# Kernel optimization log

Hardware: AMD Instinct MI355X
Metric: run time of the kernel (lower is better)

The kernel has to match this reference:

```python
import jax, jax.numpy as jnp
import numpy as np

E = 100      # embedding_dim
FS = 5       # filter_size
HS = 6       # hidden_size (conv output spatial)
D1, D2 = 10, 10  # emb_dim1, emb_dim2
RD = E * FS * FS  # relation_dim = 2500
NE = 100000  # num_entities
NR = 500     # num_relations
B = 256      # batch
EPS = 1e-5


def _bn(x, g, b, m, v, axis):
    shape = [1] * x.ndim
    shape[axis] = x.shape[axis]
    g, b, m, v = (t.reshape(shape) for t in (g, b, m, v))
    return (x - m) * jax.lax.rsqrt(v + EPS) * g + b


def setup_inputs() -> dict:
    key = jax.random.key(0)
    ks = jax.random.split(key, 24)
    def bn_params(k, n):
        k1, k2 = jax.random.split(k)
        return (jnp.ones((n,), jnp.float32),                       # gamma
                jnp.zeros((n,), jnp.float32),                      # beta
                0.1 * jax.random.normal(k1, (n,), jnp.float32),    # running mean
                jax.random.uniform(k2, (n,), jnp.float32, 0.5, 1.5))  # running var
    bn_rel = bn_params(ks[0], RD)
    bn0 = bn_params(ks[1], 1)
    bn1 = bn_params(ks[2], E)
    bn2 = bn_params(ks[3], E)
    inp = {
        'emb_e': jax.random.normal(ks[4], (NE, E), jnp.float32),
        'emb_rel': jax.random.normal(ks[5], (NR, RD), jnp.float32) * 0.1,
        'bn_rel_g': bn_rel[0], 'bn_rel_b': bn_rel[1], 'bn_rel_m': bn_rel[2], 'bn_rel_v': bn_rel[3],
        'bn0_g': bn0[0], 'bn0_b': bn0[1], 'bn0_m': bn0[2], 'bn0_v': bn0[3],
        'bn1_g': bn1[0], 'bn1_b': bn1[1], 'bn1_m': bn1[2], 'bn1_v': bn1[3],
        'fc_w': jax.random.normal(ks[6], (E * HS * HS, E), jnp.float32) / np.sqrt(E * HS * HS),
        'fc_b': jnp.zeros((E,), jnp.float32),
        'bn2_g': bn2[0], 'bn2_b': bn2[1], 'bn2_m': bn2[2], 'bn2_v': bn2[3],
        'bias': jnp.zeros((NE,), jnp.float32),
        'e1': jax.random.randint(ks[7], (B,), 0, NE),
        'rel': jax.random.randint(ks[8], (B,), 0, NR),
    }
    return inp


def reference(emb_e, emb_rel, bn_rel_g, bn_rel_b, bn_rel_m, bn_rel_v,
              bn0_g, bn0_b, bn0_m, bn0_v, bn1_g, bn1_b, bn1_m, bn1_v,
              fc_w, fc_b, bn2_g, bn2_b, bn2_m, bn2_v, bias, e1, rel):
    # entity embedding -> (B, 1, 10, 10)
    e1_emb = emb_e[e1].reshape(B, 1, D1, D2)
    # relation embedding -> per-sample conv filters
    r = emb_rel[rel]                                   # (B, 2500)
    r = _bn(r, bn_rel_g, bn_rel_b, bn_rel_m, bn_rel_v, axis=1)
    x0 = _bn(e1_emb, bn0_g, bn0_b, bn0_m, bn0_v, axis=1)
    filters = r.reshape(B, E, FS * FS)                 # (B, 100, 25)
    # per-sample dynamic-filter conv as one batched contraction over patches
    patches = jax.lax.conv_general_dilated_patches(
        x0, (FS, FS), (1, 1), 'VALID')                 # (B, 25, 6, 6)
    x = jnp.einsum('bkhw,bck->bchw', patches, filters)  # (B, 100, 6, 6)
    x = jax.nn.relu(_bn(x, bn1_g, bn1_b, bn1_m, bn1_v, axis=1))
    x = x.reshape(B, -1)                               # (B, 3600)
    x = x @ fc_w + fc_b                                # (B, 100)
    x = jax.nn.relu(_bn(x, bn2_g, bn2_b, bn2_m, bn2_v, axis=1))
    scores = x @ emb_e.T + bias                        # (B, NE)
    return jax.nn.sigmoid(scores)
```

## Files before the change

kernel.cpp:

```cpp
#include <hip/hip_runtime.h>
#include <hip/hip_bf16.h>
#include <hip/hip_fp16.h>

#define EPS 1e-5f
#define NE_ 100000
#define B_  256

typedef _Float16 half8 __attribute__((ext_vector_type(8)));
typedef float floatx16 __attribute__((ext_vector_type(16)));

#define WS_X1    0
#define WS_PART  921600
#define WS_H16   1331200

__global__ __launch_bounds__(256) void k_conv(
    const float* __restrict__ emb_e,
    const float* __restrict__ emb_rel,
    const float* __restrict__ bnr_g, const float* __restrict__ bnr_b,
    const float* __restrict__ bnr_m, const float* __restrict__ bnr_v,
    const float* __restrict__ bn0_g, const float* __restrict__ bn0_b,
    const float* __restrict__ bn0_m, const float* __restrict__ bn0_v,
    const float* __restrict__ bn1_g, const float* __restrict__ bn1_b,
    const float* __restrict__ bn1_m, const float* __restrict__ bn1_v,
    const int* __restrict__ e1, const int* __restrict__ rel,
    float* __restrict__ x1)
{
    __shared__ float x0s[100];
    __shared__ float fs[2500];

    const int b = blockIdx.x;
    const int t = threadIdx.x;
    const int ei = e1[b];
    const int ri = rel[b];

    if (t < 100) {
        float sc = bn0_g[0] * rsqrtf(bn0_v[0] + EPS);
        float sh = bn0_b[0] - bn0_m[0] * sc;
        x0s[t] = emb_e[(size_t)ei * 100 + t] * sc + sh;
    }
    for (int j = t; j < 2500; j += 256) {
        float sc = bnr_g[j] * rsqrtf(bnr_v[j] + EPS);
        fs[j] = (emb_rel[(size_t)ri * 2500 + j] - bnr_m[j]) * sc + bnr_b[j];
    }
    __syncthreads();

    for (int idx = t; idx < 3600; idx += 256) {
        int c = idx / 36;
        int p = idx - c * 36;
        int hh = p / 6, ww = p - hh * 6;
        float sum = 0.f;
        #pragma unroll
        for (int ky = 0; ky < 5; ky++) {
            #pragma unroll
            for (int kx = 0; kx < 5; kx++) {
                sum += x0s[(hh + ky) * 10 + ww + kx] * fs[c * 25 + ky * 5 + kx];
            }
        }
        float sc = bn1_g[c] * rsqrtf(bn1_v[c] + EPS);
        float y = (sum - bn1_m[c]) * sc + bn1_b[c];
        x1[(size_t)b * 3600 + idx] = fmaxf(y, 0.f);
    }
}

__global__ __launch_bounds__(256) void k_fc(
    const float* __restrict__ x1,
    const float* __restrict__ fc_w,
    float* __restrict__ partials)
{
    __shared__ float x1s[16][226];
    const int b0  = blockIdx.x * 16;
    const int ks  = blockIdx.y;
    const int kc0 = ks * 225;
    const int t = threadIdx.x;

    for (int idx = t; idx < 16 * 225; idx += 256) {
        int m = idx / 225, kk = idx - m * 225;
        x1s[m][kk] = x1[(size_t)(b0 + m) * 3600 + kc0 + kk];
    }
    __syncthreads();

    const int o  = t & 127;
    const int mg = t >> 7;
    if (o >= 100) return;

    float acc[8] = {0.f, 0.f, 0.f, 0.f, 0.f, 0.f, 0.f, 0.f};
    const float* wp = fc_w + (size_t)kc0 * 100 + o;

    for (int k0 = 0; k0 < 225; k0 += 9) {
        float wv[9];
        #pragma unroll
        for (int u = 0; u < 9; u++) wv[u] = wp[(size_t)(k0 + u) * 100];
        #pragma unroll
        for (int u = 0; u < 9; u++) {
            #pragma unroll
            for (int j = 0; j < 8; j++)
                acc[j] += x1s[mg + 2 * j][k0 + u] * wv[u];
        }
    }
    #pragma unroll
    for (int j = 0; j < 8; j++)
        partials[(size_t)ks * 25600 + (size_t)(b0 + mg + 2 * j) * 100 + o] = acc[j];
}

__global__ __launch_bounds__(256) void k_reduce(
    const float* __restrict__ partials,
    const float* __restrict__ fc_b,
    const float* __restrict__ bn2_g, const float* __restrict__ bn2_b,
    const float* __restrict__ bn2_m, const float* __restrict__ bn2_v,
    _Float16* __restrict__ h16)
{
    const int flat = blockIdx.x * 256 + threadIdx.x;
    const int b = flat / 100;
    const int o = flat - b * 100;
    float s = fc_b[o];
    #pragma unroll
    for (int ks = 0; ks < 16; ks++) s += partials[(size_t)ks * 25600 + flat];
    float sc = bn2_g[o] * rsqrtf(bn2_v[o] + EPS);
    float y = (s - bn2_m[o]) * sc + bn2_b[o];
    y = fmaxf(y, 0.f);
    h16[((o >> 3) * 256 + b) * 8 + (o & 7)] = (_Float16)y;
    if (o < 12) {
        int kp = 100 + o;
        h16[((kp >> 3) * 256 + b) * 8 + (kp & 7)] = (_Float16)0.f;
    }
}

__global__ __launch_bounds__(256) void k_scores(
    const float* __restrict__ emb_e,
    const float* __restrict__ bias,
    const _Float16* __restrict__ h16,
    float* __restrict__ out)
{
    const int t    = threadIdx.x;
    const int wave = t >> 6;
    const int lane = t & 63;
    const int l31  = lane & 31;
    const int hf   = lane >> 5;

    const int n0     = blockIdx.x * 128 + wave * 32;
    const int m_base = blockIdx.y * 128;

    const int e  = n0 + l31;
    const int el = (e < NE_) ? e : (NE_ - 1);
    const float* erow = emb_e + (size_t)el * 100;

    half8 bf[7];
    #pragma unroll
    for (int kc = 0; kc < 7; kc++) {
        const int k0 = kc * 16 + hf * 8;
        half8 h;
        if (k0 + 8 <= 100) {
            const float4 f0 = *(const float4*)(erow + k0);
            const float4 f1 = *(const float4*)(erow + k0 + 4);
            h[0] = (_Float16)f0.x; h[1] = (_Float16)f0.y;
            h[2] = (_Float16)f0.z; h[3] = (_Float16)f0.w;
            h[4] = (_Float16)f1.x; h[5] = (_Float16)f1.y;
            h[6] = (_Float16)f1.z; h[7] = (_Float16)f1.w;
        } else if (k0 < 100) {
            const float4 f0 = *(const float4*)(erow + k0);
            h[0] = (_Float16)f0.x; h[1] = (_Float16)f0.y;
            h[2] = (_Float16)f0.z; h[3] = (_Float16)f0.w;
            h[4] = (_Float16)0.f; h[5] = (_Float16)0.f;
            h[6] = (_Float16)0.f; h[7] = (_Float16)0.f;
        } else {
            #pragma unroll
            for (int j = 0; j < 8; j++) h[j] = (_Float16)0.f;
        }
        bf[kc] = h;
    }

    const half8* hA = (const half8*)h16;

    floatx16 acc[4];
    #pragma unroll
    for (int mt = 0; mt < 4; mt++)
        #pragma unroll
        for (int r = 0; r < 16; r++) acc[mt][r] = 0.f;

    #pragma unroll
    for (int mt = 0; mt < 4; mt++) {
        const int m = m_base + mt * 32 + l31;
        #pragma unroll
        for (int kc = 0; kc < 7; kc++) {
            const half8 a = hA[(kc * 2 + hf) * 256 + m];
            acc[mt] = __builtin_amdgcn_mfma_f32_32x32x16_f16(a, bf[kc], acc[mt], 0, 0, 0);
        }
    }

    if (e < NE_) {
        const float bb = bias[e];
        #pragma unroll
        for (int mt = 0; mt < 4; mt++) {
            #pragma unroll
            for (int r = 0; r < 16; r++) {
                const int row = m_base + mt * 32 + (r & 3) + 8 * (r >> 2) + 4 * hf;
                const float v = 1.f / (1.f + __expf(-(acc[mt][r] + bb)));
                out[(size_t)row * NE_ + e] = v;
            }
        }
    }
}

extern "C" void kernel_launch(void* const* d_in, const int* in_sizes, int n_in,
                              void* d_out, int out_size, void* d_ws, size_t ws_size,
                              hipStream_t stream) {
    const float* emb_e   = (const float*)d_in[0];
    const float* emb_rel = (const float*)d_in[1];
    const float* bnr_g   = (const float*)d_in[2];
    const float* bnr_b   = (const float*)d_in[3];
    const float* bnr_m   = (const float*)d_in[4];
    const float* bnr_v   = (const float*)d_in[5];
    const float* bn0_g   = (const float*)d_in[6];
    const float* bn0_b   = (const float*)d_in[7];
    const float* bn0_m   = (const float*)d_in[8];
    const float* bn0_v   = (const float*)d_in[9];
    const float* bn1_g   = (const float*)d_in[10];
    const float* bn1_b   = (const float*)d_in[11];
    const float* bn1_m   = (const float*)d_in[12];
    const float* bn1_v   = (const float*)d_in[13];
    const float* fc_w    = (const float*)d_in[14];
    const float* fc_b    = (const float*)d_in[15];
    const float* bn2_g   = (const float*)d_in[16];
    const float* bn2_b   = (const float*)d_in[17];
    const float* bn2_m   = (const float*)d_in[18];
    const float* bn2_v   = (const float*)d_in[19];
    const float* bias    = (const float*)d_in[20];
    const int* e1  = (const int*)d_in[21];
    const int* rel = (const int*)d_in[22];

    float* ws       = (float*)d_ws;
    float* x1       = ws + WS_X1;
    float* partials = ws + WS_PART;
    _Float16* h16   = (_Float16*)(ws + WS_H16);

    k_conv<<<dim3(B_), dim3(256), 0, stream>>>(
        emb_e, emb_rel,
        bnr_g, bnr_b, bnr_m, bnr_v,
        bn0_g, bn0_b, bn0_m, bn0_v,
        bn1_g, bn1_b, bn1_m, bn1_v,
        e1, rel, x1);

    k_fc<<<dim3(16, 16), dim3(256), 0, stream>>>(x1, fc_w, partials);

    k_reduce<<<dim3(100), dim3(256), 0, stream>>>(
        partials, fc_b, bn2_g, bn2_b, bn2_m, bn2_v, h16);

    k_scores<<<dim3((NE_ + 127) / 128, 2), dim3(256), 0, stream>>>(
        emb_e, bias, h16, (float*)d_out);
}
```

Measured before the change: 223.5 us.

## Use fp16 MFMA for FC layer, split conv blocks, widen score tiles

The conv kernel is split into four blocks per sample and now writes fp16 activations in an MFMA-friendly interleaved layout. A new kernel converts fc_w to fp16 on every call. The FC layer becomes an MFMA GEMM over five K splits, replacing the scalar FMA kernel. The score kernel now covers all 256 batch rows per block, so each emb_e row is loaded and converted once instead of twice, at the cost of more accumulator registers (launch bounds 256,2). Converting the weights to fp16 adds rounding error and an extra pass over fc_w.

```diff
diff --git a/kernel.cpp b/kernel.cpp
--- a/kernel.cpp
+++ b/kernel.cpp
@@ -9,9 +9,10 @@
 typedef _Float16 half8 __attribute__((ext_vector_type(8)));
 typedef float floatx16 __attribute__((ext_vector_type(16)));
 
-#define WS_X1    0
-#define WS_PART  921600
-#define WS_H16   1331200
+#define WS_X16   0
+#define WS_B16   460800
+#define WS_PART  691200
+#define WS_H16   855040
 
 __global__ __launch_bounds__(256) void k_conv(
     const float* __restrict__ emb_e,
@@ -23,12 +24,14 @@
     const float* __restrict__ bn1_g, const float* __restrict__ bn1_b,
     const float* __restrict__ bn1_m, const float* __restrict__ bn1_v,
     const int* __restrict__ e1, const int* __restrict__ rel,
-    float* __restrict__ x1)
+    _Float16* __restrict__ x16)
 {
     __shared__ float x0s[100];
-    __shared__ float fs[2500];
-
-    const int b = blockIdx.x;
+    __shared__ float fs[625];
+
+    const int bid = blockIdx.x;
+    const int b = bid >> 2;
+    const int q = bid & 3;
     const int t = threadIdx.x;
     const int ei = e1[b];
     const int ri = rel[b];
@@ -38,98 +41,50 @@
         float sh = bn0_b[0] - bn0_m[0] * sc;
         x0s[t] = emb_e[(size_t)ei * 100 + t] * sc + sh;
     }
-    for (int j = t; j < 2500; j += 256) {
+    for (int jj = t; jj < 625; jj += 256) {
+        int j = q * 625 + jj;
         float sc = bnr_g[j] * rsqrtf(bnr_v[j] + EPS);
-        fs[j] = (emb_rel[(size_t)ri * 2500 + j] - bnr_m[j]) * sc + bnr_b[j];
+        fs[jj] = (emb_rel[(size_t)ri * 2500 + j] - bnr_m[j]) * sc + bnr_b[j];
     }
     __syncthreads();
 
-    for (int idx = t; idx < 3600; idx += 256) {
-        int c = idx / 36;
-        int p = idx - c * 36;
+    for (int idx = t; idx < 900; idx += 256) {
+        int cl = idx / 36;
+        int p = idx - cl * 36;
+        int c = q * 25 + cl;
         int hh = p / 6, ww = p - hh * 6;
         float sum = 0.f;
         #pragma unroll
         for (int ky = 0; ky < 5; ky++) {
             #pragma unroll
             for (int kx = 0; kx < 5; kx++) {
-                sum += x0s[(hh + ky) * 10 + ww + kx] * fs[c * 25 + ky * 5 + kx];
+                sum += x0s[(hh + ky) * 10 + ww + kx] * fs[cl * 25 + ky * 5 + kx];
             }
         }
         float sc = bn1_g[c] * rsqrtf(bn1_v[c] + EPS);
-        float y = (sum - bn1_m[c]) * sc + bn1_b[c];
-        x1[(size_t)b * 3600 + idx] = fmaxf(y, 0.f);
-    }
+        float y = fmaxf((sum - bn1_m[c]) * sc + bn1_b[c], 0.f);
+        int k = c * 36 + p;
+        x16[(((size_t)(k >> 3)) * 256 + b) * 8 + (k & 7)] = (_Float16)y;
+    }
+}
+
+__global__ __launch_bounds__(256) void k_wprep(
+    const float* __restrict__ fc_w,
+    _Float16* __restrict__ b16)
+{
+    const int tid = blockIdx.x * 256 + threadIdx.x;
+    const int j  = tid & 7;
+    const int n  = (tid >> 3) & 127;
+    const int c8 = tid >> 10;
+    const int k  = c8 * 8 + j;
+    float v = (n < 100) ? fc_w[(size_t)k * 100 + n] : 0.f;
+    b16[tid] = (_Float16)v;
 }
 
 __global__ __launch_bounds__(256) void k_fc(
-    const float* __restrict__ x1,
-    const float* __restrict__ fc_w,
-    float* __restrict__ partials)
-{
-    __shared__ float x1s[16][226];
-    const int b0  = blockIdx.x * 16;
-    const int ks  = blockIdx.y;
-    const int kc0 = ks * 225;
-    const int t = threadIdx.x;
-
-    for (int idx = t; idx < 16 * 225; idx += 256) {
-        int m = idx / 225, kk = idx - m * 225;
-        x1s[m][kk] = x1[(size_t)(b0 + m) * 3600 + kc0 + kk];
-    }
-    __syncthreads();
-
-    const int o  = t & 127;
-    const int mg = t >> 7;
-    if (o >= 100) return;
-
-    float acc[8] = {0.f, 0.f, 0.f, 0.f, 0.f, 0.f, 0.f, 0.f};
-    const float* wp = fc_w + (size_t)kc0 * 100 + o;
-
-    for (int k0 = 0; k0 < 225; k0 += 9) {
-        float wv[9];
-        #pragma unroll
-        for (int u = 0; u < 9; u++) wv[u] = wp[(size_t)(k0 + u) * 100];
-        #pragma unroll
-        for (int u = 0; u < 9; u++) {
-            #pragma unroll
-            for (int j = 0; j < 8; j++)
-                acc[j] += x1s[mg + 2 * j][k0 + u] * wv[u];
-        }
-    }
-    #pragma unroll
-    for (int j = 0; j < 8; j++)
-        partials[(size_t)ks * 25600 + (size_t)(b0 + mg + 2 * j) * 100 + o] = acc[j];
-}
-
-__global__ __launch_bounds__(256) void k_reduce(
-    const float* __restrict__ partials,
-    const float* __restrict__ fc_b,
-    const float* __restrict__ bn2_g, const float* __restrict__ bn2_b,
-    const float* __restrict__ bn2_m, const float* __restrict__ bn2_v,
-    _Float16* __restrict__ h16)
-{
-    const int flat = blockIdx.x * 256 + threadIdx.x;
-    const int b = flat / 100;
-    const int o = flat - b * 100;
-    float s = fc_b[o];
-    #pragma unroll
-    for (int ks = 0; ks < 16; ks++) s += partials[(size_t)ks * 25600 + flat];
-    float sc = bn2_g[o] * rsqrtf(bn2_v[o] + EPS);
-    float y = (s - bn2_m[o]) * sc + bn2_b[o];
-    y = fmaxf(y, 0.f);
-    h16[((o >> 3) * 256 + b) * 8 + (o & 7)] = (_Float16)y;
-    if (o < 12) {
-        int kp = 100 + o;
-        h16[((kp >> 3) * 256 + b) * 8 + (kp & 7)] = (_Float16)0.f;
-    }
-}
-
-__global__ __launch_bounds__(256) void k_scores(
-    const float* __restrict__ emb_e,
-    const float* __restrict__ bias,
-    const _Float16* __restrict__ h16,
-    float* __restrict__ out)
+    const _Float16* __restrict__ x16,
+    const _Float16* __restrict__ b16,
+    float* __restrict__ part)
 {
     const int t    = threadIdx.x;
     const int wave = t >> 6;
@@ -137,9 +92,71 @@
     const int l31  = lane & 31;
     const int hf   = lane >> 5;
 
-    const int n0     = blockIdx.x * 128 + wave * 32;
-    const int m_base = blockIdx.y * 128;
-
+    const int mstrip = blockIdx.x;
+    const int ks     = blockIdx.y;
+    const int m      = mstrip * 32 + l31;
+    const int nbase  = wave * 32;
+
+    const half8* A  = (const half8*)x16;
+    const half8* Bp = (const half8*)b16;
+
+    floatx16 acc;
+    #pragma unroll
+    for (int r = 0; r < 16; r++) acc[r] = 0.f;
+
+    const int kc0 = ks * 45;
+    #pragma unroll 9
+    for (int kk = 0; kk < 45; kk++) {
+        const int c8 = (kc0 + kk) * 2 + hf;
+        const half8 a = A[(size_t)c8 * 256 + m];
+        const half8 b = Bp[(size_t)c8 * 128 + nbase + l31];
+        acc = __builtin_amdgcn_mfma_f32_32x32x16_f16(a, b, acc, 0, 0, 0);
+    }
+
+    const int col = nbase + l31;
+    float* pp = part + (size_t)ks * 32768;
+    #pragma unroll
+    for (int r = 0; r < 16; r++) {
+        const int row = mstrip * 32 + (r & 3) + 8 * (r >> 2) + 4 * hf;
+        pp[(size_t)row * 128 + col] = acc[r];
+    }
+}
+
+__global__ __launch_bounds__(256) void k_hprep(
+    const float* __restrict__ part,
+    const float* __restrict__ fc_b,
+    const float* __restrict__ bn2_g, const float* __restrict__ bn2_b,
+    const float* __restrict__ bn2_m, const float* __restrict__ bn2_v,
+    _Float16* __restrict__ h16)
+{
+    const int flat = blockIdx.x * 256 + threadIdx.x;
+    const int m = flat / 100;
+    const int o = flat - m * 100;
+    float s = fc_b[o];
+    #pragma unroll
+    for (int ks = 0; ks < 5; ks++) s += part[(size_t)ks * 32768 + m * 128 + o];
+    float sc = bn2_g[o] * rsqrtf(bn2_v[o] + EPS);
+    float y = fmaxf((s - bn2_m[o]) * sc + bn2_b[o], 0.f);
+    h16[((o >> 3) * 256 + m) * 8 + (o & 7)] = (_Float16)y;
+    if (o < 12) {
+        int kp = 100 + o;
+        h16[((kp >> 3) * 256 + m) * 8 + (kp & 7)] = (_Float16)0.f;
+    }
+}
+
+__global__ __launch_bounds__(256, 2) void k_scores(
+    const float* __restrict__ emb_e,
+    const float* __restrict__ bias,
+    const _Float16* __restrict__ h16,
+    float* __restrict__ out)
+{
+    const int t    = threadIdx.x;
+    const int wave = t >> 6;
+    const int lane = t & 63;
+    const int l31  = lane & 31;
+    const int hf   = lane >> 5;
+
+    const int n0 = blockIdx.x * 128 + wave * 32;
     const int e  = n0 + l31;
     const int el = (e < NE_) ? e : (NE_ - 1);
     const float* erow = emb_e + (size_t)el * 100;
@@ -164,22 +181,23 @@
             h[6] = (_Float16)0.f; h[7] = (_Float16)0.f;
         } else {
             #pragma unroll
-            for (int j = 0; j < 8; j++) h[j] = (_Float16)0.f;
+            for (int jj = 0; jj < 8; jj++) h[jj] = (_Float16)0.f;
         }
         bf[kc] = h;
     }
 
     const half8* hA = (const half8*)h16;
-
-    floatx16 acc[4];
-    #pragma unroll
-    for (int mt = 0; mt < 4; mt++)
+    const float bb = bias[el];
+
+    floatx16 acc[8];
+    #pragma unroll
+    for (int mt = 0; mt < 8; mt++)
         #pragma unroll
         for (int r = 0; r < 16; r++) acc[mt][r] = 0.f;
 
     #pragma unroll
-    for (int mt = 0; mt < 4; mt++) {
-        const int m = m_base + mt * 32 + l31;
+    for (int mt = 0; mt < 8; mt++) {
+        const int m = mt * 32 + l31;
         #pragma unroll
         for (int kc = 0; kc < 7; kc++) {
             const half8 a = hA[(kc * 2 + hf) * 256 + m];
@@ -188,14 +206,12 @@
     }
 
     if (e < NE_) {
-        const float bb = bias[e];
-        #pragma unroll
-        for (int mt = 0; mt < 4; mt++) {
+        #pragma unroll
+        for (int mt = 0; mt < 8; mt++) {
             #pragma unroll
             for (int r = 0; r < 16; r++) {
-                const int row = m_base + mt * 32 + (r & 3) + 8 * (r >> 2) + 4 * hf;
-                const float v = 1.f / (1.f + __expf(-(acc[mt][r] + bb)));
-                out[(size_t)row * NE_ + e] = v;
+                const int row = mt * 32 + (r & 3) + 8 * (r >> 2) + 4 * hf;
+                out[(size_t)row * NE_ + e] = 1.f / (1.f + __expf(-(acc[mt][r] + bb)));
             }
         }
     }
@@ -228,23 +244,26 @@
     const int* e1  = (const int*)d_in[21];
     const int* rel = (const int*)d_in[22];
 
-    float* ws       = (float*)d_ws;
-    float* x1       = ws + WS_X1;
-    float* partials = ws + WS_PART;
-    _Float16* h16   = (_Float16*)(ws + WS_H16);
-
-    k_conv<<<dim3(B_), dim3(256), 0, stream>>>(
+    float* ws = (float*)d_ws;
+    _Float16* x16 = (_Float16*)(ws + WS_X16);
+    _Float16* b16 = (_Float16*)(ws + WS_B16);
+    float*    prt = ws + WS_PART;
+    _Float16* h16 = (_Float16*)(ws + WS_H16);
+
+    k_conv<<<dim3(1024), dim3(256), 0, stream>>>(
         emb_e, emb_rel,
         bnr_g, bnr_b, bnr_m, bnr_v,
         bn0_g, bn0_b, bn0_m, bn0_v,
         bn1_g, bn1_b, bn1_m, bn1_v,
-        e1, rel, x1);
-
-    k_fc<<<dim3(16, 16), dim3(256), 0, stream>>>(x1, fc_w, partials);
-
-    k_reduce<<<dim3(100), dim3(256), 0, stream>>>(
-        partials, fc_b, bn2_g, bn2_b, bn2_m, bn2_v, h16);
-
-    k_scores<<<dim3((NE_ + 127) / 128, 2), dim3(256), 0, stream>>>(
+        e1, rel, x16);
+
+    k_wprep<<<dim3(1800), dim3(256), 0, stream>>>(fc_w, b16);
+
+    k_fc<<<dim3(8, 5), dim3(256), 0, stream>>>(x16, b16, prt);
+
+    k_hprep<<<dim3(100), dim3(256), 0, stream>>>(
+        prt, fc_b, bn2_g, bn2_b, bn2_m, bn2_v, h16);
+
+    k_scores<<<dim3((NE_ + 127) / 128), dim3(256), 0, stream>>>(
         emb_e, bias, h16, (float*)d_out);
 }
```

Result: no change. 226.0 us (+1.1%).
